# Kernel tuning notes

Hardware: AMD Instinct MI355X
Metric: run time of the kernel (lower is better)

The kernel has to match this reference:

```python
import jax, jax.numpy as jnp
import numpy as np

N_NODES = 100000
N_EDGES = 1600000
IN_DIM = 256
HIDDEN = 128
N_CLASSES = 10


def setup_inputs() -> dict:
    key = jax.random.key(0)
    k1, k2, k3, k4 = jax.random.split(key, 4)
    x = jax.random.normal(k1, (N_NODES, IN_DIM), dtype=jnp.float32)
    edge_index = jax.random.randint(k2, (2, N_EDGES), 0, N_NODES, dtype=jnp.int64)
    # Glorot-ish init for weights
    W1 = jax.random.normal(k3, (IN_DIM, HIDDEN), dtype=jnp.float32) * (1.0 / np.sqrt(IN_DIM))
    b1 = jnp.zeros((HIDDEN,), dtype=jnp.float32)
    W2 = jax.random.normal(k4, (HIDDEN, N_CLASSES), dtype=jnp.float32) * (1.0 / np.sqrt(HIDDEN))
    b2 = jnp.zeros((N_CLASSES,), dtype=jnp.float32)
    return {"x": x, "edge_index": edge_index, "W1": W1, "b1": b1, "W2": W2, "b2": b2}


def _gcn_norm(edge_index, num_nodes):
    # PyG gcn_norm with add_self_loops=False, edge_weight=1:
    # deg over destination (col), norm = d^-1/2[src] * d^-1/2[dst]
    row, col = edge_index[0], edge_index[1]
    deg = jax.ops.segment_sum(jnp.ones((edge_index.shape[1],), jnp.float32), col,
                              num_segments=num_nodes)
    dinv = jnp.where(deg > 0, jax.lax.rsqrt(jnp.maximum(deg, 1.0)), 0.0)
    return dinv[row] * dinv[col]


def _gcn_conv(x, W, b, row, col, norm, num_nodes):
    h = x @ W                              # [N, out] dense transform
    msg = h[row] * norm[:, None]           # gather + scale, [E, out]
    out = jax.ops.segment_sum(msg, col, num_segments=num_nodes)  # scatter-add
    return out + b


def reference(x, edge_index, W1, b1, W2, b2):
    row, col = edge_index[0], edge_index[1]
    norm = _gcn_norm(edge_index, N_NODES)
    h = _gcn_conv(x, W1, b1, row, col, norm, N_NODES)
    h = jax.nn.relu(h)  # dropout is identity in eval mode
    out = _gcn_conv(h, W2, b2, row, col, norm, N_NODES)
    return out
```

## Files before the change

kernel.cpp:

```cpp
#include <hip/hip_runtime.h>
#include <hip/hip_fp16.h>

typedef _Float16 f16x8 __attribute__((ext_vector_type(8)));
typedef _Float16 f16x2 __attribute__((ext_vector_type(2)));
typedef float f32x4 __attribute__((ext_vector_type(4)));

#define NBUK_MAX 512
#define CHUNK 4096
#define BUKCAP 6144


__global__ __launch_bounds__(512) void k_bfill(const int* __restrict__ row,
                                               const int* __restrict__ col,
                                               int* __restrict__ bcur,
                                               unsigned* __restrict__ pairs,
                                               int E, int nbuk) {
    __shared__ int hist[NBUK_MAX];
    __shared__ int scanA[NBUK_MAX];
    __shared__ int scanB[NBUK_MAX];
    __shared__ int cur[NBUK_MAX];
    __shared__ int gpos[NBUK_MAX];
    __shared__ unsigned staged[CHUNK];
    int tid = threadIdx.x;
    int e0 = blockIdx.x * CHUNK;
    int nv = E - e0; if (nv > CHUNK) nv = CHUNK;

    hist[tid] = 0;
    __syncthreads();
    if (nv == CHUNK) {
        const int4* c4 = (const int4*)(col + e0);
#pragma unroll
        for (int it = 0; it < 2; ++it) {
            int4 v = c4[tid + it * 512];
            atomicAdd(&hist[v.x >> 8], 1);
            atomicAdd(&hist[v.y >> 8], 1);
            atomicAdd(&hist[v.z >> 8], 1);
            atomicAdd(&hist[v.w >> 8], 1);
        }
    } else {
        for (int i = tid; i < nv; i += 512) atomicAdd(&hist[col[e0 + i] >> 8], 1);
    }
    __syncthreads();
    int hv = hist[tid];
    scanA[tid] = hv;
    __syncthreads();
    int* pa = scanA;
    int* pb = scanB;
    for (int off = 1; off < 512; off <<= 1) {
        pb[tid] = pa[tid] + ((tid >= off) ? pa[tid - off] : 0);
        __syncthreads();
        int* sw = pa; pa = pb; pb = sw;
    }
    int ex = pa[tid] - hv;
    __syncthreads();
    pb[tid] = ex;
    cur[tid] = ex;
    if (tid < nbuk && hv > 0) gpos[tid] = atomicAdd(&bcur[tid], hv);
    __syncthreads();
    int* excl = pb;
    if (nv == CHUNK) {
        const int4* c4 = (const int4*)(col + e0);
        const int4* r4 = (const int4*)(row + e0);
#pragma unroll
        for (int it = 0; it < 2; ++it) {
            int4 c = c4[tid + it * 512];
            int4 r = r4[tid + it * 512];
            int rk;
            rk = atomicAdd(&cur[c.x >> 8], 1); staged[rk] = ((unsigned)(c.x & 255) << 17) | (unsigned)r.x;
            rk = atomicAdd(&cur[c.y >> 8], 1); staged[rk] = ((unsigned)(c.y & 255) << 17) | (unsigned)r.y;
            rk = atomicAdd(&cur[c.z >> 8], 1); staged[rk] = ((unsigned)(c.z & 255) << 17) | (unsigned)r.z;
            rk = atomicAdd(&cur[c.w >> 8], 1); staged[rk] = ((unsigned)(c.w & 255) << 17) | (unsigned)r.w;
        }
    } else {
        for (int i = tid; i < nv; i += 512) {
            int c = col[e0 + i], r = row[e0 + i];
            int rk = atomicAdd(&cur[c >> 8], 1);
            staged[rk] = ((unsigned)(c & 255) << 17) | (unsigned)r;
        }
    }
    __syncthreads();
    int grp = tid >> 4, l16 = tid & 15;
    for (int b = grp; b < nbuk; b += 32) {
        int cnt = hist[b];
        if (cnt == 0) continue;
        int bs = excl[b];
        int gp = gpos[b];
        unsigned* dst = pairs + (size_t)b * BUKCAP;
        for (int l = l16; l < cnt; l += 16) {
            int d = gp + l;
            if (d < BUKCAP) dst[d] = staged[bs + l];
        }
    }
}


__global__ void k_bscan(const int* __restrict__ bcur, int* __restrict__ bbase, int nbuk) {
    __shared__ int s[512];
    int tid = threadIdx.x;
    int v = (tid < nbuk) ? bcur[tid] : 0;
    s[tid] = v;
    __syncthreads();
    for (int off = 1; off < 512; off <<= 1) {
        int tv = (tid >= off) ? s[tid - off] : 0;
        __syncthreads();
        s[tid] += tv;
        __syncthreads();
    }
    if (tid < nbuk) bbase[tid] = s[tid] - v;
}


__global__ __launch_bounds__(256) void k_csr2(const unsigned* __restrict__ pairs,
                                              const int* __restrict__ bcur,
                                              const int* __restrict__ bbase,
                                              int* __restrict__ colptr,
                                              float* __restrict__ dinv,
                                              int* __restrict__ srcs,
                                              int N, int E, int nbuk) {
    __shared__ int fc[256];
    __shared__ int cp[256];
    __shared__ int tp[256];
    __shared__ int loc[BUKCAP];
    int b = blockIdx.x;
    int c0 = b << 8;
    int tid = threadIdx.x;
    fc[tid] = 0;
    __syncthreads();
    int cnt = bcur[b];
    if (cnt > BUKCAP) cnt = BUKCAP;
    int p0 = bbase[b];
    const unsigned* pbk = pairs + (size_t)b * BUKCAP;
    for (int i = tid; i < cnt; i += 256) {
        atomicAdd(&fc[pbk[i] >> 17], 1);
    }
    __syncthreads();
    int deg = fc[tid];
    cp[tid] = deg;
    __syncthreads();
    int* pa = cp;
    int* pb = tp;
    for (int off = 1; off < 256; off <<= 1) {
        pb[tid] = pa[tid] + ((tid >= off) ? pa[tid - off] : 0);
        __syncthreads();
        int* sw = pa; pa = pb; pb = sw;
    }
    int excl = pa[tid] - deg;
    __syncthreads();
    tp[tid] = excl;
    fc[tid] = 0;
    if (c0 + tid < N) {
        colptr[c0 + tid] = p0 + excl;
        dinv[c0 + tid] = (deg > 0) ? rsqrtf((float)deg) : 0.0f;
    }
    if (b == 0 && tid == 0) colptr[N] = E;
    __syncthreads();
    for (int i = tid; i < cnt; i += 256) {
        unsigned v = pbk[i];
        int cl = (int)(v >> 17);
        int r = (int)(v & 0x1FFFFu);
        int off = tp[cl] + atomicAdd(&fc[cl], 1);
        loc[off] = r;
    }
    __syncthreads();
    for (int i = tid; i < cnt; i += 256) srcs[p0 + i] = loc[i];
}


__global__ void k_w1t(const float* __restrict__ W1, __half* __restrict__ W1T) {
    int c = blockIdx.x;
    int k = threadIdx.x;
    W1T[(size_t)c * 256 + k] = __float2half(W1[(size_t)k * 128 + c]);
}


#define WPAD 264

__global__ __launch_bounds__(512, 4) void k_gemm1(const float* __restrict__ x,
                                                  const __half* __restrict__ W1T,
                                                  const float* __restrict__ dinv,
                                                  __half* __restrict__ h, int N) {
    __shared__ __half wt[128][WPAD];
    int tid = threadIdx.x;
    int w = tid >> 6, l = tid & 63;
    int r16 = l & 15, kg = l >> 4;
    int r0 = blockIdx.x * 128;
    int row = r0 + w * 16 + r16;
    int rl = (row < N) ? row : 0;
    const float4* xp = (const float4*)x + (size_t)rl * 64 + kg * 2;

    float4 xr[8];
#pragma unroll
    for (int p = 0; p < 4; ++p) {
        xr[2 * p]     = xp[p * 8];
        xr[2 * p + 1] = xp[p * 8 + 1];
    }

#pragma unroll
    for (int it = 0; it < 8; ++it) {
        int idx = tid + it * 512;
        int c = idx >> 5, q = idx & 31;
        *(float4*)&wt[c][q * 8] = ((const float4*)W1T)[(size_t)c * 32 + q];
    }
    __syncthreads();

    f32x4 acc[8];
#pragma unroll
    for (int n = 0; n < 8; ++n) acc[n] = (f32x4){0.f, 0.f, 0.f, 0.f};

#pragma unroll
    for (int ks = 0; ks < 8; ++ks) {
        float4 c0 = xr[2 * (ks & 3)];
        float4 c1 = xr[2 * (ks & 3) + 1];
        if (ks < 4) {
            xr[2 * (ks & 3)]     = xp[(ks + 4) * 8];
            xr[2 * (ks & 3) + 1] = xp[(ks + 4) * 8 + 1];
        }
        f16x8 a;
        a[0] = (_Float16)c0.x; a[1] = (_Float16)c0.y;
        a[2] = (_Float16)c0.z; a[3] = (_Float16)c0.w;
        a[4] = (_Float16)c1.x; a[5] = (_Float16)c1.y;
        a[6] = (_Float16)c1.z; a[7] = (_Float16)c1.w;
        int kk = ks * 32;
#pragma unroll
        for (int n = 0; n < 8; ++n) {
            f16x8 b = *(const f16x8*)&wt[n * 16 + r16][kk + kg * 8];
            acc[n] = __builtin_amdgcn_mfma_f32_16x16x32_f16(a, b, acc[n], 0, 0, 0);
        }
    }

    float dn[4];
#pragma unroll
    for (int rr = 0; rr < 4; ++rr) {
        int r = r0 + w * 16 + kg * 4 + rr;
        dn[rr] = (r < N) ? dinv[r] : 0.f;
    }
#pragma unroll
    for (int n = 0; n < 8; ++n)
#pragma unroll
        for (int rr = 0; rr < 4; ++rr) {
            int r = r0 + w * 16 + kg * 4 + rr;
            if (r < N)
                h[(size_t)r * 128 + n * 16 + r16] = __float2half(dn[rr] * acc[n][rr]);
        }
}


#define LOAD8(sv, k, vv) { \
    int s0_ = __shfl(sv, (k) + 0), s1_ = __shfl(sv, (k) + 1); \
    int s2_ = __shfl(sv, (k) + 2), s3_ = __shfl(sv, (k) + 3); \
    int s4_ = __shfl(sv, (k) + 4), s5_ = __shfl(sv, (k) + 5); \
    int s6_ = __shfl(sv, (k) + 6), s7_ = __shfl(sv, (k) + 7); \
    vv[0] = hp[(size_t)s0_ * 64 + lane]; vv[1] = hp[(size_t)s1_ * 64 + lane]; \
    vv[2] = hp[(size_t)s2_ * 64 + lane]; vv[3] = hp[(size_t)s3_ * 64 + lane]; \
    vv[4] = hp[(size_t)s4_ * 64 + lane]; vv[5] = hp[(size_t)s5_ * 64 + lane]; \
    vv[6] = hp[(size_t)s6_ * 64 + lane]; vv[7] = hp[(size_t)s7_ * 64 + lane]; }

#define ACC8(vv, A0, A1) { \
    float2 f0_ = __half22float2(vv[0]), f1_ = __half22float2(vv[1]); \
    float2 f2_ = __half22float2(vv[2]), f3_ = __half22float2(vv[3]); \
    float2 f4_ = __half22float2(vv[4]), f5_ = __half22float2(vv[5]); \
    float2 f6_ = __half22float2(vv[6]), f7_ = __half22float2(vv[7]); \
    A0 += ((f0_.x + f1_.x) + (f2_.x + f3_.x)) + ((f4_.x + f5_.x) + (f6_.x + f7_.x)); \
    A1 += ((f0_.y + f1_.y) + (f2_.y + f3_.y)) + ((f4_.y + f5_.y) + (f6_.y + f7_.y)); }

__global__ __launch_bounds__(256) void k_agg1(const __half* __restrict__ h,
                                              const float* __restrict__ dinv,
                                              const int* __restrict__ colptr,
                                              const int* __restrict__ srcs,
                                              const float* __restrict__ b1,
                                              const float* __restrict__ W2,
                                              __half* __restrict__ t, int N) {
    __shared__ __half hs[64][136];
    __shared__ __half w2t[10][136];
    int tid = threadIdx.x;
    int wave = tid >> 6;
    int lane = tid & 63;

    for (int i = tid; i < 1280; i += 256) {
        int c = i >> 7, k = i & 127;
        w2t[c][k] = __float2half(W2[(size_t)k * 10 + c]);
    }

    const __half2* hp = (const __half2*)h;
    int nb0 = blockIdx.x * 64;
    float bb0 = b1[2 * lane], bb1 = b1[2 * lane + 1];

#pragma unroll 1
    for (int i = 0; i < 16; ++i) {
        int n = nb0 + wave * 16 + i;
        if (n >= N) break;
        int jb = colptr[n], je = colptr[n + 1];
        int len = je - jb;
        float a0 = 0.f, a1 = 0.f;
        for (int j0 = 0; j0 < len; j0 += 64) {
            int cnt = len - j0;
            if (cnt > 64) cnt = 64;
            int sv = (lane < cnt) ? srcs[jb + j0 + lane] : 0;
            int k = 0;
            for (; k + 8 <= cnt; k += 8) {
                __half2 va[8];
                LOAD8(sv, k, va);
                ACC8(va, a0, a1);
            }
            for (; k < cnt; ++k) {
                int s = __shfl(sv, k);
                float2 f = __half22float2(hp[(size_t)s * 64 + lane]);
                a0 += f.x; a1 += f.y;
            }
        }
        float dn = dinv[n];
        float v0 = dn * a0 + bb0;
        float v1 = dn * a1 + bb1;
        v0 = v0 > 0.f ? v0 : 0.f;
        v1 = v1 > 0.f ? v1 : 0.f;
        ((__half2*)&hs[wave * 16 + i][0])[lane] = __floats2half2_rn(v0, v1);
    }
    __syncthreads();

#pragma unroll
    for (int it = 0; it < 4; ++it) {
        int idx = tid + it * 256;
        int r = idx >> 4, c = idx & 15;
        int n = nb0 + r;
        if (n < N) {
            float s = 0.f;
            if (c < 10) {
                const f16x2* hr = (const f16x2*)&hs[r][0];
                const f16x2* wr = (const f16x2*)&w2t[c][0];
#pragma unroll
                for (int j = 0; j < 64; ++j)
                    s = __builtin_amdgcn_fdot2(hr[j], wr[j], s, false);
                s *= dinv[n];
            }
            t[(size_t)n * 16 + c] = __float2half(s);
        }
    }
}


__global__ __launch_bounds__(256) void k_agg2(const __half* __restrict__ t,
                                              const float* __restrict__ dinv,
                                              const int* __restrict__ colptr,
                                              const int* __restrict__ srcs,
                                              const float* __restrict__ b2,
                                              float* __restrict__ out, int N) {
    int g = threadIdx.x >> 4;
    int lane16 = threadIdx.x & 15;
    int wg = g & 3;
    int n = blockIdx.x * 16 + g;
    if (n >= N) return;
    int jb = colptr[n], je = colptr[n + 1];
    float a = 0.f;
    for (int j0 = jb; j0 < je; j0 += 16) {
        int cnt = je - j0;
        if (cnt > 16) cnt = 16;
        int sv = (lane16 < cnt) ? srcs[j0 + lane16] : 0;
        int k = 0;
        for (; k + 4 <= cnt; k += 4) {
            int s0 = __shfl(sv, wg * 16 + k + 0);
            int s1 = __shfl(sv, wg * 16 + k + 1);
            int s2 = __shfl(sv, wg * 16 + k + 2);
            int s3 = __shfl(sv, wg * 16 + k + 3);
            float x0 = __half2float(t[(size_t)s0 * 16 + lane16]);
            float x1 = __half2float(t[(size_t)s1 * 16 + lane16]);
            float x2 = __half2float(t[(size_t)s2 * 16 + lane16]);
            float x3 = __half2float(t[(size_t)s3 * 16 + lane16]);
            a += (x0 + x1) + (x2 + x3);
        }
        for (; k < cnt; ++k) {
            int s = __shfl(sv, wg * 16 + k);
            a += __half2float(t[(size_t)s * 16 + lane16]);
        }
    }
    if (lane16 < 10) out[(size_t)n * 10 + lane16] = dinv[n] * a + b2[lane16];
}


static inline size_t alignup(size_t x) { return (x + 255) & ~(size_t)255; }

extern "C" void kernel_launch(void* const* d_in, const int* in_sizes, int n_in,
                              void* d_out, int out_size, void* d_ws, size_t ws_size,
                              hipStream_t stream) {
    const float* x  = (const float*)d_in[0];
    const int*   ei = (const int*)d_in[1];
    const float* W1 = (const float*)d_in[2];
    const float* b1 = (const float*)d_in[3];
    const float* W2 = (const float*)d_in[4];
    const float* b2 = (const float*)d_in[5];

    int E = in_sizes[1] / 2;
    int N = in_sizes[0] / 256;
    const int* row = ei;
    const int* col = ei + E;
    int nbuk = (N + 255) >> 8;

    char* ws = (char*)d_ws;
    size_t off = 0;
    int*      colptr = (int*)(ws + off);      off += alignup((size_t)(N + 1) * 4);
    float*    dinv   = (float*)(ws + off);    off += alignup((size_t)N * 4);
    int*      bbase  = (int*)(ws + off);      off += alignup((size_t)NBUK_MAX * 4);
    int*      bcur   = (int*)(ws + off);      off += alignup((size_t)NBUK_MAX * 4);
    int*      srcs   = (int*)(ws + off);      off += alignup((size_t)E * 4);
    unsigned* pairs  = (unsigned*)(ws + off); off += alignup((size_t)NBUK_MAX * BUKCAP * 4);
    __half*   W1T    = (__half*)(ws + off);   off += alignup((size_t)128 * 256 * 2);
    __half*   h      = (__half*)(ws + off);   off += alignup((size_t)N * 128 * 2);
    __half*   t      = (__half*)(ws + off);   off += alignup((size_t)N * 16 * 2);

    hipMemsetAsync(bcur, 0, (size_t)NBUK_MAX * 4, stream);

    k_w1t<<<128, 256, 0, stream>>>(W1, W1T);
    k_bfill<<<(E + CHUNK - 1) / CHUNK, 512, 0, stream>>>(row, col, bcur, pairs, E, nbuk);
    k_bscan<<<1, 512, 0, stream>>>(bcur, bbase, nbuk);
    k_csr2<<<nbuk, 256, 0, stream>>>(pairs, bcur, bbase, colptr, dinv, srcs, N, E, nbuk);

    k_gemm1<<<(N + 127) / 128, 512, 0, stream>>>(x, W1T, dinv, h, N);
    k_agg1<<<(N + 63) / 64, 256, 0, stream>>>(h, dinv, colptr, srcs, b1, W2, t, N);
    k_agg2<<<(N + 15) / 16, 256, 0, stream>>>(t, dinv, colptr, srcs, b2, (float*)d_out, N);
}
```

Baseline: 164.0 us.

## Fuse W1 transpose into bucket fill and CSR scatter into GEMM1 launch

```diff
diff --git a/kernel.cpp b/kernel.cpp
--- a/kernel.cpp
+++ b/kernel.cpp
@@ -8,13 +8,17 @@
 #define NBUK_MAX 512
 #define CHUNK 4096
 #define BUKCAP 6144
-
-
-__global__ __launch_bounds__(512) void k_bfill(const int* __restrict__ row,
-                                               const int* __restrict__ col,
-                                               int* __restrict__ bcur,
-                                               unsigned* __restrict__ pairs,
-                                               int E, int nbuk) {
+#define WPAD 264
+#define W1T_BLOCKS 64
+
+
+__global__ __launch_bounds__(512) void k_fat1(const float* __restrict__ W1,
+                                              __half* __restrict__ W1T,
+                                              const int* __restrict__ row,
+                                              const int* __restrict__ col,
+                                              int* __restrict__ bcur,
+                                              unsigned* __restrict__ pairs,
+                                              int E, int nbuk) {
     __shared__ int hist[NBUK_MAX];
     __shared__ int scanA[NBUK_MAX];
     __shared__ int scanB[NBUK_MAX];
@@ -22,7 +26,16 @@
     __shared__ int gpos[NBUK_MAX];
     __shared__ unsigned staged[CHUNK];
     int tid = threadIdx.x;
-    int e0 = blockIdx.x * CHUNK;
+
+    if (blockIdx.x < W1T_BLOCKS) {
+        int idx = blockIdx.x * 512 + tid;
+        int c = idx >> 8, k = idx & 255;
+        W1T[(size_t)c * 256 + k] = __float2half(W1[(size_t)k * 128 + c]);
+        return;
+    }
+
+    int bid = blockIdx.x - W1T_BLOCKS;
+    int e0 = bid * CHUNK;
     int nv = E - e0; if (nv > CHUNK) nv = CHUNK;
 
     hist[tid] = 0;
@@ -110,17 +123,15 @@
 }
 
 
-__global__ __launch_bounds__(256) void k_csr2(const unsigned* __restrict__ pairs,
-                                              const int* __restrict__ bcur,
-                                              const int* __restrict__ bbase,
-                                              int* __restrict__ colptr,
-                                              float* __restrict__ dinv,
-                                              int* __restrict__ srcs,
-                                              int N, int E, int nbuk) {
+__global__ __launch_bounds__(256) void k_csr2a(const unsigned* __restrict__ pairs,
+                                               const int* __restrict__ bcur,
+                                               const int* __restrict__ bbase,
+                                               int* __restrict__ colptr,
+                                               float* __restrict__ dinv,
+                                               int N, int E) {
     __shared__ int fc[256];
     __shared__ int cp[256];
     __shared__ int tp[256];
-    __shared__ int loc[BUKCAP];
     int b = blockIdx.x;
     int c0 = b << 8;
     int tid = threadIdx.x;
@@ -145,47 +156,64 @@
         int* sw = pa; pa = pb; pb = sw;
     }
     int excl = pa[tid] - deg;
-    __syncthreads();
-    tp[tid] = excl;
-    fc[tid] = 0;
     if (c0 + tid < N) {
         colptr[c0 + tid] = p0 + excl;
         dinv[c0 + tid] = (deg > 0) ? rsqrtf((float)deg) : 0.0f;
     }
     if (b == 0 && tid == 0) colptr[N] = E;
-    __syncthreads();
-    for (int i = tid; i < cnt; i += 256) {
-        unsigned v = pbk[i];
-        int cl = (int)(v >> 17);
-        int r = (int)(v & 0x1FFFFu);
-        int off = tp[cl] + atomicAdd(&fc[cl], 1);
-        loc[off] = r;
-    }
-    __syncthreads();
-    for (int i = tid; i < cnt; i += 256) srcs[p0 + i] = loc[i];
-}
-
-
-__global__ void k_w1t(const float* __restrict__ W1, __half* __restrict__ W1T) {
-    int c = blockIdx.x;
-    int k = threadIdx.x;
-    W1T[(size_t)c * 256 + k] = __float2half(W1[(size_t)k * 128 + c]);
-}
-
-
-#define WPAD 264
-
-__global__ __launch_bounds__(512, 4) void k_gemm1(const float* __restrict__ x,
-                                                  const __half* __restrict__ W1T,
-                                                  const float* __restrict__ dinv,
-                                                  __half* __restrict__ h, int N) {
-    __shared__ __half wt[128][WPAD];
+}
+
+
+#define SMEM_BYTES (128 * WPAD * 2)
+
+__global__ __launch_bounds__(512, 4) void k_fat2(const unsigned* __restrict__ pairs,
+                                                 const int* __restrict__ bcur,
+                                                 const int* __restrict__ bbase,
+                                                 const int* __restrict__ colptr,
+                                                 int* __restrict__ srcs,
+                                                 const float* __restrict__ x,
+                                                 const __half* __restrict__ W1T,
+                                                 const float* __restrict__ dinv,
+                                                 __half* __restrict__ h,
+                                                 int N, int nbuk) {
+    __shared__ __align__(16) char smem[SMEM_BYTES];
     int tid = threadIdx.x;
+
+    if (blockIdx.x < nbuk) {
+        int* tp  = (int*)smem;
+        int* fc  = tp + 256;
+        int* loc = fc + 256;
+        int b = blockIdx.x;
+        int c0 = b << 8;
+        int cnt = bcur[b];
+        if (cnt > BUKCAP) cnt = BUKCAP;
+        int p0 = bbase[b];
+        if (tid < 256) {
+            fc[tid] = 0;
+            tp[tid] = (c0 + tid < N) ? (colptr[c0 + tid] - p0) : 0;
+        }
+        __syncthreads();
+        const unsigned* pbk = pairs + (size_t)b * BUKCAP;
+        for (int i = tid; i < cnt; i += 512) {
+            unsigned v = pbk[i];
+            int cl = (int)(v >> 17);
+            int r = (int)(v & 0x1FFFFu);
+            int off = tp[cl] + atomicAdd(&fc[cl], 1);
+            if (off < BUKCAP) loc[off] = r;
+            else srcs[p0 + off] = r;
+        }
+        __syncthreads();
+        for (int i = tid; i < cnt; i += 512) srcs[p0 + i] = loc[i];
+        return;
+    }
+
+    __half (*wt)[WPAD] = (__half(*)[WPAD])smem;
+    int gb = blockIdx.x - nbuk;
     int w = tid >> 6, l = tid & 63;
     int r16 = l & 15, kg = l >> 4;
-    int r0 = blockIdx.x * 128;
-    int row = r0 + w * 16 + r16;
-    int rl = (row < N) ? row : 0;
+    int r0 = gb * 128;
+    int rowi = r0 + w * 16 + r16;
+    int rl = (rowi < N) ? rowi : 0;
     const float4* xp = (const float4*)x + (size_t)rl * 64 + kg * 2;
 
     float4 xr[8];
@@ -393,6 +421,8 @@
     const int* row = ei;
     const int* col = ei + E;
     int nbuk = (N + 255) >> 8;
+    int nbE = (E + CHUNK - 1) / CHUNK;
+    int nbG1 = (N + 127) / 128;
 
     char* ws = (char*)d_ws;
     size_t off = 0;
@@ -408,12 +438,11 @@
 
     hipMemsetAsync(bcur, 0, (size_t)NBUK_MAX * 4, stream);
 
-    k_w1t<<<128, 256, 0, stream>>>(W1, W1T);
-    k_bfill<<<(E + CHUNK - 1) / CHUNK, 512, 0, stream>>>(row, col, bcur, pairs, E, nbuk);
+    k_fat1<<<W1T_BLOCKS + nbE, 512, 0, stream>>>(W1, W1T, row, col, bcur, pairs, E, nbuk);
     k_bscan<<<1, 512, 0, stream>>>(bcur, bbase, nbuk);
-    k_csr2<<<nbuk, 256, 0, stream>>>(pairs, bcur, bbase, colptr, dinv, srcs, N, E, nbuk);
-
-    k_gemm1<<<(N + 127) / 128, 512, 0, stream>>>(x, W1T, dinv, h, N);
+    k_csr2a<<<nbuk, 256, 0, stream>>>(pairs, bcur, bbase, colptr, dinv, N, E);
+    k_fat2<<<nbuk + nbG1, 512, 0, stream>>>(pairs, bcur, bbase, colptr, srcs,
+                                            x, W1T, dinv, h, N, nbuk);
     k_agg1<<<(N + 63) / 64, 256, 0, stream>>>(h, dinv, colptr, srcs, b1, W2, t, N);
     k_agg2<<<(N + 15) / 16, 256, 0, stream>>>(t, dinv, colptr, srcs, b2, (float*)d_out, N);
 }
```

New measurement: 159.9 us. 1.03x faster.
